# Performance work log

Measured on AMD Instinct MI355X. Metric: run time of the kernel, lower is better.

The kernel has to match this reference:

```python
import jax, jax.numpy as jnp
import numpy as np

B, INPUTDIM, OUTDIM, GRIDSIZE = 4096, 128, 512, 300

def setup_inputs() -> dict:
    key = jax.random.key(0)
    k1, k2 = jax.random.split(key)
    x = jax.random.normal(k1, (B, INPUTDIM), dtype=jnp.float32)
    scale = 1.0 / (np.sqrt(INPUTDIM) * np.sqrt(GRIDSIZE))
    fouriercoeffs = jax.random.normal(k2, (2, OUTDIM, INPUTDIM, GRIDSIZE), dtype=jnp.float32) * scale
    return {"x": x, "fouriercoeffs": fouriercoeffs}

def reference(x, fouriercoeffs):
    # k: frequencies 1..gridsize
    gridsize = fouriercoeffs.shape[-1]
    k = jnp.arange(1, gridsize + 1, dtype=x.dtype)  # (G,)
    arg = x[:, :, None] * k  # (B, I, G)
    c = jnp.cos(arg)
    s = jnp.sin(arg)
    # einsum('dbik,djik->bj') with d=2 split into cos/sin terms
    y = jnp.einsum('big,jig->bj', c, fouriercoeffs[0]) + jnp.einsum('big,jig->bj', s, fouriercoeffs[1])
    return y
```

## Files before the change

### kernel.cpp

```cpp
#include <hip/hip_runtime.h>
#include <hip/hip_bf16.h>
#include <cstdint>

#define TB 256

typedef short short8 __attribute__((ext_vector_type(8)));
typedef float f32x4 __attribute__((ext_vector_type(4)));

constexpr int B_N = 4096, I_N = 128, J_N = 512, G_N = 300;
constexpr int K1 = I_N * G_N;
constexpr int BM = 128, BN = 256;
constexpr int NSP = 8;
constexpr int IC = 16;
constexpr float INV2PI = 0.15915494309189535f;

constexpr int GSTRIDE = 4 * 512 * 8;
constexpr size_t SPSTRIDE = (size_t)G_N * GSTRIDE;

__device__ __forceinline__ ushort f2bf(float f) {
    unsigned int u = __float_as_uint(f);
    return (ushort)((u + 0x7FFFu + ((u >> 16) & 1u)) >> 16);
}

__device__ __forceinline__ float fract_(float x) {
#if __has_builtin(__builtin_amdgcn_fractf)
    return __builtin_amdgcn_fractf(x);
#else
    return x - floorf(x);
#endif
}

__device__ __forceinline__ unsigned int pack_bf2(float a, float b) {
    __hip_bfloat162 h = __float22bfloat162_rn(make_float2(a, b));
    unsigned int u;
    __builtin_memcpy(&u, &h, 4);
    return u;
}

typedef __attribute__((address_space(3))) unsigned int lds_u32_t;
typedef __attribute__((address_space(1))) const unsigned int glb_u32_t;

__device__ __forceinline__ void llds16(const void* g, void* l) {
    __builtin_amdgcn_global_load_lds(
        reinterpret_cast<glb_u32_t*>(reinterpret_cast<uintptr_t>(g)),
        reinterpret_cast<lds_u32_t*>((unsigned int)reinterpret_cast<uintptr_t>(l)),
        16, 0, 0);
}

constexpr int TRG = 60;
constexpr int TRTB = 512;
constexpr int TRUNITS = 256 * 15;

__global__ __launch_bounds__(TRTB) void fkan_tr(const float* __restrict__ src,
                                                ushort* __restrict__ dst,
                                                float* __restrict__ outz) {
    __shared__ __align__(16) ushort L[TRG * 2 * 32 * 8];
    const int gc = blockIdx.x;
    const int sp = blockIdx.y;
    const int djc = blockIdx.z;
    const int dj0 = djc * 32;
    const int d = dj0 >> 9;
    const int j0 = dj0 & 511;
    const int g0 = gc * TRG;
    const int tid = threadIdx.x;

    {
        size_t bid = (size_t)(djc * 8 + sp) * 5 + gc;
        size_t zt = bid * TRTB + tid;
        if (zt < (size_t)B_N * J_N / 4)
            ((float4*)outz)[zt] = make_float4(0.f, 0.f, 0.f, 0.f);
    }

    unsigned int* Lw = (unsigned int*)L;

    auto rbody = [&](int u) {
        int rp = u / 15, c = u - rp * 15;
        int djl = rp >> 3, ilp = rp & 7;
        int ihl = ilp >> 2, e2 = ilp & 3;
        const float* p = src + ((size_t)(dj0 + djl) * 128 + sp * 16 + ilp * 2) * 300
                       + g0 + c * 4;
        float4 va = *(const float4*)p;
        float4 vb = *(const float4*)(p + 300);
        float a[4] = {va.x, va.y, va.z, va.w};
        float b[4] = {vb.x, vb.y, vb.z, vb.w};
        const int swz = (c & 7) << 2;
#pragma unroll
        for (int k = 0; k < 4; ++k) {
            int gl = c * 4 + k;
            int wd = ((gl * 2 + ihl) * 32 + djl) * 4 + e2;
            Lw[wd ^ swz] = pack_bf2(a[k], b[k]);
        }
    };
#pragma unroll
    for (int it = 0; it < 7; ++it) rbody(tid + it * TRTB);
    if (tid < TRUNITS - 7 * TRTB) rbody(tid + 7 * TRTB);
    __syncthreads();

    const uint4* Lv = (const uint4*)L;
    auto wbody = [&](int w) {
        int gl = w >> 6, r = w & 63;
        int ihl = r >> 5, jl = r & 31;
        int q = (gl * 64 + ihl * 32 + jl) ^ ((gl >> 2) & 7);
        size_t d16 = ((size_t)(sp * G_N + g0 + gl) * 4 + d * 2 + ihl) * 512 + j0 + jl;
        ((uint4*)dst)[d16] = Lv[q];
    };
#pragma unroll
    for (int it = 0; it < 7; ++it) wbody(tid + it * TRTB);
    if (tid < TRG * 64 - 7 * TRTB) wbody(tid + 7 * TRTB);
}

__global__ __launch_bounds__(TB, 2)
void fkan_gemm(const float* __restrict__ x,
               const ushort* __restrict__ fcb,
               float* __restrict__ out) {
    __shared__ __align__(16) ushort At[2 * 4 * 128 * 8];
    __shared__ __align__(16) ushort Bt[2 * 4 * 256 * 8];

    const int tid = threadIdx.x;
    const int bm = blockIdx.x, bn = blockIdx.y, sp = blockIdx.z;
    const int lane = tid & 63, wid = tid >> 6;
    const int wm = wid & 1, wn = wid >> 1;
    const int lhi = lane >> 4, llo = lane & 15;
    const int m = tid & 127, half = tid >> 7;

    float sv[8], cv[8], s0[8], c0[8];
    {
        const float* xr = x + ((size_t)(bm * BM + m)) * I_N + sp * IC + half * 8;
        float4 xa = *(const float4*)xr;
        float4 xb = *(const float4*)(xr + 4);
        float xv[8] = {xa.x, xa.y, xa.z, xa.w, xb.x, xb.y, xb.z, xb.w};
#pragma unroll
        for (int j = 0; j < 8; ++j) {
            float r = fract_(xv[j] * INV2PI);
            s0[j] = __builtin_amdgcn_sinf(r);
            c0[j] = __builtin_amdgcn_cosf(r);
            sv[j] = s0[j];
            cv[j] = c0[j];
        }
    }

    const ushort* bp[4];
#pragma unroll
    for (int q = 0; q < 4; ++q)
        bp[q] = fcb + (size_t)sp * SPSTRIDE
              + ((size_t)wid * 512 + bn * BN + q * 64 + lane) * 8;

    const int aoff = (lhi * 128 + wm * 64 + llo) * 8;
    const int boff = (lhi * 256 + wn * 128 + llo) * 8;
    ushort* awc0 = &At[(half * 128 + m) * 8];
    ushort* aws0 = &At[((2 + half) * 128 + m) * 8];

    f32x4 acc[4][8];
#pragma unroll
    for (int a = 0; a < 4; ++a)
#pragma unroll
        for (int b = 0; b < 8; ++b) acc[a][b] = (f32x4){0.f, 0.f, 0.f, 0.f};

    auto stageB = [&](int nb) {
#pragma unroll
        for (int q = 0; q < 4; ++q) {
            llds16(bp[q], (char*)Bt + (size_t)(nb * 1024 + wid * 256 + q * 64) * 16);
            bp[q] += GSTRIDE;
        }
    };
    auto writeA = [&](int nb) {
        uint4 vc = {pack_bf2(cv[0], cv[1]), pack_bf2(cv[2], cv[3]),
                    pack_bf2(cv[4], cv[5]), pack_bf2(cv[6], cv[7])};
        *(uint4*)(awc0 + nb * 4096) = vc;
        uint4 vs = {pack_bf2(sv[0], sv[1]), pack_bf2(sv[2], sv[3]),
                    pack_bf2(sv[4], sv[5]), pack_bf2(sv[6], sv[7])};
        *(uint4*)(aws0 + nb * 4096) = vs;
#pragma unroll
        for (int j = 0; j < 8; ++j) {
            float t = __builtin_fmaf(sv[j], c0[j], cv[j] * s0[j]);
            cv[j] = __builtin_fmaf(cv[j], c0[j], -(sv[j] * s0[j]));
            sv[j] = t;
        }
    };
    auto halfstep = [&](int cb, bool doNext) {
        __syncthreads();
        if (doNext) stageB(cb ^ 1);
        short8 af[4], bfr[8];
#pragma unroll
        for (int t = 0; t < 4; ++t)
            af[t] = *(const short8*)&At[cb * 4096 + aoff + t * 128];
#pragma unroll
        for (int t = 0; t < 8; ++t)
            bfr[t] = *(const short8*)&Bt[cb * 8192 + boff + t * 128];
#pragma unroll
        for (int tm = 0; tm < 4; ++tm)
#pragma unroll
            for (int tn = 0; tn < 8; ++tn)
                acc[tm][tn] = __builtin_amdgcn_mfma_f32_16x16x32_bf16(
                    af[tm], bfr[tn], acc[tm][tn], 0, 0, 0);
        if (doNext) writeA(cb ^ 1);
    };

    writeA(0);
    stageB(0);

    for (int g = 0; g < G_N; g += 2) {
        halfstep(0, true);
        halfstep(1, g + 2 < G_N);
    }

    const int row0 = bm * BM + wm * 64 + lhi * 4;
    const int col0 = bn * BN + wn * 128 + llo;
#pragma unroll
    for (int tm = 0; tm < 4; ++tm)
#pragma unroll
        for (int tn = 0; tn < 8; ++tn)
#pragma unroll
            for (int r = 0; r < 4; ++r)
                atomicAdd(&out[(size_t)(row0 + tm * 16 + r) * J_N + col0 + tn * 16],
                          acc[tm][tn][r]);
}

constexpr int SPL_FB = 4;
constexpr int KS_FB = 2 * K1 / SPL_FB;
constexpr int NSTEP_FB = KS_FB / 32;

__global__ __launch_bounds__(TB)
void fkan_gemm_fb(const float* __restrict__ x,
                  const float* __restrict__ fc32,
                  float* __restrict__ out) {
    __shared__ float xs[BM][65];
    __shared__ __align__(16) ushort At[4 * 128 * 8];
    __shared__ __align__(16) ushort Bt[4 * 128 * 8];

    const int tid = threadIdx.x;
    const int bm = blockIdx.x, bn = blockIdx.y, sp = blockIdx.z;
    const int d = sp >> 1;
    const int ib = (sp & 1) << 6;
    const int rbase = ib * G_N;

    for (int idx = tid; idx < BM * 64; idx += TB) {
        int row = idx >> 6, il = idx & 63;
        xs[row][il] = x[(size_t)(bm * BM + row) * I_N + ib + il];
    }

    f32x4 acc[4][4];
#pragma unroll
    for (int a = 0; a < 4; ++a)
#pragma unroll
        for (int b = 0; b < 4; ++b) acc[a][b] = (f32x4){0.f, 0.f, 0.f, 0.f};

    const int lane = tid & 63, wid = tid >> 6;
    const int wm = wid & 1, wn = wid >> 1;
    const int lhi = lane >> 4, llo = lane & 15;
    const int am = tid & 127, akg0 = tid >> 7;

    const float* f32base = fc32 + ((size_t)d * J_N + bn * 128) * K1 + rbase;

    for (int step = 0; step < NSTEP_FB; ++step) {
        __syncthreads();
#pragma unroll
        for (int it = 0; it < 2; ++it) {
            const int kg = akg0 + it * 2;
            int r = rbase + step * 32 + kg * 8;
            int i = (int)((unsigned)r / 300u);
            int g = r - i * 300;
            float xxv = xs[am][i - ib];
            float kkf = (float)(g + 1);
            short8 avv;
#pragma unroll
            for (int j = 0; j < 8; ++j) {
                float rev = xxv * kkf * INV2PI;
                float fr = fract_(rev) + (d ? 0.0f : 0.25f);
                avv[j] = (short)f2bf(__builtin_amdgcn_sinf(fract_(fr)));
                if (j < 7) {
                    ++g; kkf += 1.0f;
                    if (g == 300) { g = 0; kkf = 1.0f; ++i; xxv = xs[am][i - ib]; }
                }
            }
            *(short8*)&At[(kg * 128 + am) * 8] = avv;
        }
#pragma unroll
        for (int it = 0; it < 2; ++it) {
            int item = tid + it * TB;
            int n = item >> 2, grp = item & 3;
            const float* gp = f32base + (size_t)n * K1 + step * 32 + grp * 8;
            float4 v0 = *(const float4*)gp;
            float4 v1 = *(const float4*)(gp + 4);
            short8 bv;
            bv[0] = (short)f2bf(v0.x); bv[1] = (short)f2bf(v0.y);
            bv[2] = (short)f2bf(v0.z); bv[3] = (short)f2bf(v0.w);
            bv[4] = (short)f2bf(v1.x); bv[5] = (short)f2bf(v1.y);
            bv[6] = (short)f2bf(v1.z); bv[7] = (short)f2bf(v1.w);
            *(short8*)&Bt[(grp * 128 + n) * 8] = bv;
        }
        __syncthreads();
        short8 af[4], bf[4];
#pragma unroll
        for (int t = 0; t < 4; ++t) {
            af[t] = *(const short8*)&At[(lhi * 128 + wm * 64 + t * 16 + llo) * 8];
            bf[t] = *(const short8*)&Bt[(lhi * 128 + wn * 64 + t * 16 + llo) * 8];
        }
#pragma unroll
        for (int tm = 0; tm < 4; ++tm)
#pragma unroll
            for (int tn = 0; tn < 4; ++tn)
                acc[tm][tn] = __builtin_amdgcn_mfma_f32_16x16x32_bf16(
                    af[tm], bf[tn], acc[tm][tn], 0, 0, 0);
    }

    const int row0 = bm * BM + wm * 64 + lhi * 4;
    const int col0 = bn * 128 + wn * 64 + llo;
#pragma unroll
    for (int tm = 0; tm < 4; ++tm)
#pragma unroll
        for (int tn = 0; tn < 4; ++tn)
#pragma unroll
            for (int r = 0; r < 4; ++r)
                atomicAdd(&out[(size_t)(row0 + tm * 16 + r) * J_N + col0 + tn * 16],
                          acc[tm][tn][r]);
}

extern "C" void kernel_launch(void* const* d_in, const int* in_sizes, int n_in,
                              void* d_out, int out_size, void* d_ws, size_t ws_size,
                              hipStream_t stream) {
    const float* x = (const float*)d_in[0];
    const float* fc = (const float*)d_in[1];
    float* out = (float*)d_out;

    const size_t need = (size_t)2 * J_N * K1 * sizeof(ushort);

    if (ws_size >= need) {
        ushort* fcb = (ushort*)d_ws;
        fkan_tr<<<dim3(5, 8, 32), TRTB, 0, stream>>>(fc, fcb, out);
        dim3 grid(B_N / BM, J_N / BN, NSP);
        fkan_gemm<<<grid, TB, 0, stream>>>(x, fcb, out);
    } else {
        hipMemsetAsync(d_out, 0, (size_t)out_size * sizeof(float), stream);
        dim3 grid(B_N / BM, J_N / 128, SPL_FB);
        fkan_gemm_fb<<<grid, TB, 0, stream>>>(x, fc, out);
    }
}
```

Measured before the change: 530.8 us.

## Widen GEMM block to full output width with 512 threads per block

The main GEMM block now covers all 512 output columns with 8 waves instead of splitting the columns across two blocks. The sin/cos generation of the A tile is therefore computed once per row block rather than once per column block. The B prefetch is moved after the LDS fragment reads. The cost is twice the LDS footprint for B, half as many blocks in the grid (256 instead of 512), and 512-thread blocks that may lower occupancy.

```diff
diff --git a/kernel.cpp b/kernel.cpp
--- a/kernel.cpp
+++ b/kernel.cpp
@@ -3,13 +3,14 @@
 #include <cstdint>
 
 #define TB 256
+#define TBG 512
 
 typedef short short8 __attribute__((ext_vector_type(8)));
 typedef float f32x4 __attribute__((ext_vector_type(4)));
 
 constexpr int B_N = 4096, I_N = 128, J_N = 512, G_N = 300;
 constexpr int K1 = I_N * G_N;
-constexpr int BM = 128, BN = 256;
+constexpr int BM = 128, BN = 512;
 constexpr int NSP = 8;
 constexpr int IC = 16;
 constexpr float INV2PI = 0.15915494309189535f;
@@ -109,28 +110,28 @@
     if (tid < TRG * 64 - 7 * TRTB) wbody(tid + 7 * TRTB);
 }
 
-__global__ __launch_bounds__(TB, 2)
+__global__ __launch_bounds__(TBG, 2)
 void fkan_gemm(const float* __restrict__ x,
                const ushort* __restrict__ fcb,
                float* __restrict__ out) {
     __shared__ __align__(16) ushort At[2 * 4 * 128 * 8];
-    __shared__ __align__(16) ushort Bt[2 * 4 * 256 * 8];
+    __shared__ __align__(16) ushort Bt[2 * 4 * 512 * 8];
 
     const int tid = threadIdx.x;
-    const int bm = blockIdx.x, bn = blockIdx.y, sp = blockIdx.z;
+    const int bm = blockIdx.x, sp = blockIdx.z;
     const int lane = tid & 63, wid = tid >> 6;
     const int wm = wid & 1, wn = wid >> 1;
     const int lhi = lane >> 4, llo = lane & 15;
-    const int m = tid & 127, half = tid >> 7;
-
-    float sv[8], cv[8], s0[8], c0[8];
+    const int m = tid & 127, q4 = tid >> 7;
+    const int ihq = q4 >> 1, eq = (q4 & 1) * 4;
+
+    float sv[4], cv[4], s0[4], c0[4];
     {
-        const float* xr = x + ((size_t)(bm * BM + m)) * I_N + sp * IC + half * 8;
+        const float* xr = x + ((size_t)(bm * BM + m)) * I_N + sp * IC + q4 * 4;
         float4 xa = *(const float4*)xr;
-        float4 xb = *(const float4*)(xr + 4);
-        float xv[8] = {xa.x, xa.y, xa.z, xa.w, xb.x, xb.y, xb.z, xb.w};
-#pragma unroll
-        for (int j = 0; j < 8; ++j) {
+        float xv[4] = {xa.x, xa.y, xa.z, xa.w};
+#pragma unroll
+        for (int j = 0; j < 4; ++j) {
             float r = fract_(xv[j] * INV2PI);
             s0[j] = __builtin_amdgcn_sinf(r);
             c0[j] = __builtin_amdgcn_cosf(r);
@@ -141,14 +142,14 @@
 
     const ushort* bp[4];
 #pragma unroll
-    for (int q = 0; q < 4; ++q)
-        bp[q] = fcb + (size_t)sp * SPSTRIDE
-              + ((size_t)wid * 512 + bn * BN + q * 64 + lane) * 8;
+    for (int p = 0; p < 4; ++p)
+        bp[p] = fcb + (size_t)sp * SPSTRIDE
+              + ((size_t)((wid >> 1) * 512 + (wid & 1) * 256 + p * 64 + lane)) * 8;
 
     const int aoff = (lhi * 128 + wm * 64 + llo) * 8;
-    const int boff = (lhi * 256 + wn * 128 + llo) * 8;
-    ushort* awc0 = &At[(half * 128 + m) * 8];
-    ushort* aws0 = &At[((2 + half) * 128 + m) * 8];
+    const int boff = (lhi * 512 + wn * 128 + llo) * 8;
+    ushort* awc0 = &At[(ihq * 128 + m) * 8 + eq];
+    ushort* aws0 = &At[((2 + ihq) * 128 + m) * 8 + eq];
 
     f32x4 acc[4][8];
 #pragma unroll
@@ -158,20 +159,19 @@
 
     auto stageB = [&](int nb) {
 #pragma unroll
-        for (int q = 0; q < 4; ++q) {
-            llds16(bp[q], (char*)Bt + (size_t)(nb * 1024 + wid * 256 + q * 64) * 16);
-            bp[q] += GSTRIDE;
+        for (int p = 0; p < 4; ++p) {
+            llds16(bp[p], (char*)Bt
+                       + (size_t)(nb * 2048 + (wid >> 1) * 512 + (wid & 1) * 256 + p * 64) * 16);
+            bp[p] += GSTRIDE;
         }
     };
     auto writeA = [&](int nb) {
-        uint4 vc = {pack_bf2(cv[0], cv[1]), pack_bf2(cv[2], cv[3]),
-                    pack_bf2(cv[4], cv[5]), pack_bf2(cv[6], cv[7])};
-        *(uint4*)(awc0 + nb * 4096) = vc;
-        uint4 vs = {pack_bf2(sv[0], sv[1]), pack_bf2(sv[2], sv[3]),
-                    pack_bf2(sv[4], sv[5]), pack_bf2(sv[6], sv[7])};
-        *(uint4*)(aws0 + nb * 4096) = vs;
-#pragma unroll
-        for (int j = 0; j < 8; ++j) {
+        uint2 vc = {pack_bf2(cv[0], cv[1]), pack_bf2(cv[2], cv[3])};
+        *(uint2*)(awc0 + nb * 4096) = vc;
+        uint2 vs = {pack_bf2(sv[0], sv[1]), pack_bf2(sv[2], sv[3])};
+        *(uint2*)(aws0 + nb * 4096) = vs;
+#pragma unroll
+        for (int j = 0; j < 4; ++j) {
             float t = __builtin_fmaf(sv[j], c0[j], cv[j] * s0[j]);
             cv[j] = __builtin_fmaf(cv[j], c0[j], -(sv[j] * s0[j]));
             sv[j] = t;
@@ -179,14 +179,14 @@
     };
     auto halfstep = [&](int cb, bool doNext) {
         __syncthreads();
-        if (doNext) stageB(cb ^ 1);
         short8 af[4], bfr[8];
 #pragma unroll
         for (int t = 0; t < 4; ++t)
             af[t] = *(const short8*)&At[cb * 4096 + aoff + t * 128];
 #pragma unroll
         for (int t = 0; t < 8; ++t)
-            bfr[t] = *(const short8*)&Bt[cb * 8192 + boff + t * 128];
+            bfr[t] = *(const short8*)&Bt[cb * 16384 + boff + t * 128];
+        if (doNext) stageB(cb ^ 1);
 #pragma unroll
         for (int tm = 0; tm < 4; ++tm)
 #pragma unroll
@@ -205,7 +205,7 @@
     }
 
     const int row0 = bm * BM + wm * 64 + lhi * 4;
-    const int col0 = bn * BN + wn * 128 + llo;
+    const int col0 = wn * 128 + llo;
 #pragma unroll
     for (int tm = 0; tm < 4; ++tm)
 #pragma unroll
@@ -224,7 +224,7 @@
 void fkan_gemm_fb(const float* __restrict__ x,
                   const float* __restrict__ fc32,
                   float* __restrict__ out) {
-    __shared__ float xs[BM][65];
+    __shared__ float xs[128][65];
     __shared__ __align__(16) ushort At[4 * 128 * 8];
     __shared__ __align__(16) ushort Bt[4 * 128 * 8];
 
@@ -234,9 +234,9 @@
     const int ib = (sp & 1) << 6;
     const int rbase = ib * G_N;
 
-    for (int idx = tid; idx < BM * 64; idx += TB) {
+    for (int idx = tid; idx < 128 * 64; idx += TB) {
         int row = idx >> 6, il = idx & 63;
-        xs[row][il] = x[(size_t)(bm * BM + row) * I_N + ib + il];
+        xs[row][il] = x[(size_t)(bm * 128 + row) * I_N + ib + il];
     }
 
     f32x4 acc[4][4];
@@ -304,7 +304,7 @@
                     af[tm], bf[tn], acc[tm][tn], 0, 0, 0);
     }
 
-    const int row0 = bm * BM + wm * 64 + lhi * 4;
+    const int row0 = bm * 128 + wm * 64 + lhi * 4;
     const int col0 = bn * 128 + wn * 64 + llo;
 #pragma unroll
     for (int tm = 0; tm < 4; ++tm)
@@ -328,11 +328,11 @@
     if (ws_size >= need) {
         ushort* fcb = (ushort*)d_ws;
         fkan_tr<<<dim3(5, 8, 32), TRTB, 0, stream>>>(fc, fcb, out);
-        dim3 grid(B_N / BM, J_N / BN, NSP);
-        fkan_gemm<<<grid, TB, 0, stream>>>(x, fcb, out);
+        dim3 grid(B_N / BM, 1, NSP);
+        fkan_gemm<<<grid, TBG, 0, stream>>>(x, fcb, out);
     } else {
         hipMemsetAsync(d_out, 0, (size_t)out_size * sizeof(float), stream);
-        dim3 grid(B_N / BM, J_N / 128, SPL_FB);
+        dim3 grid(B_N / 128, J_N / 128, SPL_FB);
         fkan_gemm_fb<<<grid, TB, 0, stream>>>(x, fc, out);
     }
 }
```

Result: no change. 528.8 us (-0.4%).
